# Kernel tuning notes

Hardware: AMD Instinct MI355X
Metric: run time of the kernel (lower is better)

## Reference

```python
import jax, jax.numpy as jnp
import numpy as np

K = 32  # neighbors per query point


def _gather_points(x, idx):
    # x: [B, N, D], idx: [B, M, k] -> [B, M, k, D]
    B, M, k = idx.shape
    D = x.shape[-1]
    flat = jnp.take_along_axis(x, idx.reshape(B, M * k, 1), axis=1)
    return flat.reshape(B, M, k, D)


def setup_inputs() -> dict:
    key = jax.random.key(0)
    k1, k2, k3, k4, k5 = jax.random.split(key, 5)
    B, N, M, Cin = 16, 4096, 1024, 64
    pos = jax.random.normal(k1, (B, N, 3), dtype=jnp.float32)
    features = jax.random.normal(k2, (B, N, Cin), dtype=jnp.float32)
    idx = jax.random.randint(k3, (B, M), 0, N, dtype=jnp.int64)
    # 1x1 conv2d MLP params: (Cin+3) -> 64 -> 128 (use_xyz adds 3 channels)
    W1 = jax.random.normal(k4, (Cin + 3, 64), dtype=jnp.float32) * (1.0 / np.sqrt(Cin + 3))
    b1 = jnp.zeros((64,), dtype=jnp.float32)
    W2 = jax.random.normal(k5, (64, 128), dtype=jnp.float32) * (1.0 / np.sqrt(64))
    b2 = jnp.zeros((128,), dtype=jnp.float32)
    return {"pos": pos, "features": features, "W1": W1, "b1": b1,
            "W2": W2, "b2": b2, "idx": idx}


def reference(pos, features, W1, b1, W2, b2, idx):
    # pos: [B,N,3], features: [B,N,C], idx: [B,M] query-point indices
    pos_q = jnp.take_along_axis(pos, idx[..., None], axis=1)  # [B,M,3]
    # squared-distance knn: [B,M,N]
    d2 = (jnp.sum(pos_q ** 2, -1, keepdims=True)
          + jnp.sum(pos ** 2, -1)[:, None, :]
          - 2.0 * jnp.einsum("bmd,bnd->bmn", pos_q, pos))
    _, nn_idx = jax.lax.top_k(-d2, K)  # [B,M,K] nearest neighbors
    grouped_pos = _gather_points(pos, nn_idx)          # [B,M,K,3]
    grouped_feat = _gather_points(features, nn_idx)    # [B,M,K,C]
    rel = grouped_pos - pos_q[:, :, None, :]           # recenter groups
    x = jnp.concatenate([rel, grouped_feat], axis=-1)  # [B,M,K,C+3] (use_xyz)
    # 1x1 conv2d MLP == per-point linear + ReLU on channel dim
    h = jax.nn.relu(jnp.einsum("bmkc,cd->bmkd", x, W1) + b1)
    h = jax.nn.relu(jnp.einsum("bmkc,cd->bmkd", h, W2) + b2)
    out = jnp.max(h, axis=-2)  # max over K neighbors -> [B,M,128]
    return (pos_q, out)
```

## Files before the change

kernel.cpp:

```cpp
#include <hip/hip_runtime.h>

#define NPTS  4096
#define MQ    1024
#define BATCH 16
#define KNN   32
#define CIN   64
#define H1D   64
#define H2D   128

typedef _Float16 half8 __attribute__((ext_vector_type(8)));
typedef float    floatx4 __attribute__((ext_vector_type(4)));

#define WS_NN_BYTES ((size_t)BATCH * MQ * KNN * 4)
#define W1F_HALVES  (3 * 4 * 64 * 8)
#define W2F_HALVES  (2 * 8 * 64 * 8)
#define WS_P4_OFF   (WS_NN_BYTES + (W1F_HALVES + W2F_HALVES) * 2)

__global__ __launch_bounds__(256) void wprep_kernel(
    const float* __restrict__ W1, const float* __restrict__ W2,
    const float* __restrict__ pos,
    _Float16* __restrict__ wout, float4* __restrict__ pos4)
{
    const int gid = blockIdx.x * 256 + threadIdx.x;
    if (gid < 768) {
        const int s = gid;
        const int kc = s >> 8, nt = (s >> 6) & 3, lane = s & 63;
        const int col = lane & 15, quad = lane >> 4;
        half8 ph;
#pragma unroll
        for (int j = 0; j < 8; ++j) {
            const int k = kc * 32 + quad * 8 + j;
            ph[j] = (k < 67) ? (_Float16)W1[k * H1D + nt * 16 + col] : (_Float16)0.0f;
        }
        *(half8*)(wout + (size_t)s * 8) = ph;
    } else if (gid < 1792) {
        const int s2 = gid - 768;
        const int kc2 = s2 >> 9, nt2 = (s2 >> 6) & 7, lane = s2 & 63;
        const int col = lane & 15, quad = lane >> 4;
        half8 ph;
#pragma unroll
        for (int j = 0; j < 8; ++j) {
            const int k = kc2 * 32 + quad * 8 + j;
            ph[j] = (_Float16)W2[k * H2D + nt2 * 16 + col];
        }
        *(half8*)(wout + (size_t)W1F_HALVES + (size_t)s2 * 8) = ph;
    } else {
        const int p = gid - 1792;
        if (p < BATCH * NPTS) {
            const float px = pos[p * 3 + 0], py = pos[p * 3 + 1], pz = pos[p * 3 + 2];
            float4 v;
            v.x = px; v.y = py; v.z = pz;
            v.w = __fadd_rn(__fadd_rn(__fmul_rn(px, px), __fmul_rn(py, py)),
                            __fmul_rn(pz, pz));
            pos4[p] = v;
        }
    }
}

__global__ __launch_bounds__(256, 4) void knn_kernel(
    const float4* __restrict__ pos4, const int* __restrict__ idx,
    float* __restrict__ pos_q, int* __restrict__ nn)
{
    const int bid = blockIdx.x;
    const int b   = bid >> 10;
    const int m   = bid & (MQ - 1);
    const int t   = threadIdx.x;
    const int wv  = t >> 6, lane = t & 63;

    __shared__ __align__(16) unsigned int hist[1024];
    __shared__ unsigned int wred[8];
    __shared__ unsigned int wsum[4];
    __shared__ unsigned int sc[8];
    __shared__ unsigned int ckey[64];
    __shared__ int          cidx[64];
    __shared__ int          outidx[KNN];

    const float4* pb4 = pos4 + (size_t)b * NPTS;
    const int qn = idx[(size_t)b * MQ + m];
    const float4 qv = pb4[qn];
    const float qq = qv.w;

    *(uint4*)&hist[t * 4] = make_uint4(0u, 0u, 0u, 0u);

    float4 p[16];
#pragma unroll
    for (int i = 0; i < 16; ++i) p[i] = pb4[i * 256 + t];

    unsigned int k[16];
    unsigned int lmin = 0xFFFFFFFFu, lmax = 0u;
#pragma unroll
    for (int i = 0; i < 16; ++i) {
        const float qp = __fadd_rn(__fadd_rn(__fmul_rn(qv.x, p[i].x), __fmul_rn(qv.y, p[i].y)),
                                   __fmul_rn(qv.z, p[i].z));
        const float d2 = __fsub_rn(__fadd_rn(qq, p[i].w), __fmul_rn(2.0f, qp));
        unsigned int u = __float_as_uint(d2);
        u = (u & 0x80000000u) ? ~u : (u | 0x80000000u);
        k[i] = u;
        lmin = min(lmin, u);
        lmax = max(lmax, u);
    }
#pragma unroll
    for (int off = 32; off; off >>= 1) {
        lmin = min(lmin, (unsigned int)__shfl_xor(lmin, off));
        lmax = max(lmax, (unsigned int)__shfl_xor(lmax, off));
    }
    if (lane == 0) { wred[wv] = lmin; wred[4 + wv] = lmax; }
    __syncthreads();
    const unsigned int umin = min(min(wred[0], wred[1]), min(wred[2], wred[3]));
    const unsigned int umax = max(max(wred[4], wred[5]), max(wred[6], wred[7]));
    const unsigned int rng  = umax - umin;
#pragma unroll
    for (int i = 0; i < 16; ++i) k[i] -= umin;

    int sCur;
    {
        const int bits = (rng == 0u) ? 0 : (32 - __clz(rng));
        sCur = (bits > 10) ? (bits - 10) : 0;
    }

#pragma unroll
    for (int i = 0; i < 16; ++i) atomicAdd(&hist[k[i] >> sCur], 1u);
    __syncthreads();

    unsigned int prefix = 0u, rank = KNN - 1;
    int bcnt = 0, nb = 0;
    bool first = true;
    for (;;) {
        const uint4 c4 = *(const uint4*)&hist[t * 4];
        const unsigned int ssum = c4.x + c4.y + c4.z + c4.w;
        unsigned int v = ssum;
#pragma unroll
        for (int off = 1; off < 64; off <<= 1) {
            const unsigned int o = __shfl_up(v, off);
            if (lane >= off) v += o;
        }
        if (lane == 63) wsum[wv] = v;
        __syncthreads();
        unsigned int woff = 0;
        for (int i = 0; i < wv; ++i) woff += wsum[i];
        const unsigned int incl = woff + v, excl = incl - ssum;
        if (rank >= excl && rank < incl) {
            const unsigned int cnt[4] = {c4.x, c4.y, c4.z, c4.w};
            unsigned int e = excl;
            for (int j = 0; j < 4; ++j) {
                if (rank < e + cnt[j]) {
                    sc[0] = (unsigned int)(t * 4 + j);
                    sc[1] = rank - e;
                    sc[2] = cnt[j];
                    break;
                }
                e += cnt[j];
            }
        }
        __syncthreads();
        const unsigned int bin = sc[0];
        rank = sc[1];
        bcnt = (int)sc[2];
        prefix = first ? bin : ((prefix << nb) | bin);
        first = false;
        if (bcnt <= 64 || sCur == 0) break;

        const int sNext = (sCur > 10) ? (sCur - 10) : 0;
        nb = sCur - sNext;
        __syncthreads();
        *(uint4*)&hist[t * 4] = make_uint4(0u, 0u, 0u, 0u);
        __syncthreads();
        const unsigned int mask = (1u << nb) - 1u;
#pragma unroll
        for (int i = 0; i < 16; ++i) {
            if ((k[i] >> sCur) == prefix)
                atomicAdd(&hist[(k[i] >> sNext) & mask], 1u);
        }
        __syncthreads();
        sCur = sNext;
    }

    if (t == 0) { sc[3] = 0u; sc[4] = 0u; }
    __syncthreads();
#pragma unroll
    for (int i = 0; i < 16; ++i) {
        const unsigned int hp = k[i] >> sCur;
        if (hp < prefix) {
            outidx[atomicAdd(&sc[3], 1u)] = i * 256 + t;
        } else if (hp == prefix) {
            const unsigned int slot = atomicAdd(&sc[4], 1u);
            if (slot < 64u) { ckey[slot] = k[i]; cidx[slot] = i * 256 + t; }
        }
    }
    __syncthreads();
    const int defcnt  = (int)sc[3];
    const int candcnt = min((int)sc[4], 64);

    if (wv == 0) {
        const unsigned int k_l = (lane < candcnt) ? ckey[lane] : 0xFFFFFFFFu;
        const int          i_l = (lane < candcnt) ? cidx[lane] : 0x7FFFFFFF;
        int rk = 0;
        for (int j = 0; j < candcnt; ++j) {
            const unsigned int kj = __shfl(k_l, j);
            const int          ij = __shfl(i_l, j);
            if (kj < k_l || (kj == k_l && ij < i_l)) ++rk;
        }
        if (lane < candcnt && rk <= (int)rank) outidx[defcnt + rk] = i_l;
    }
    __syncthreads();
    if (t < KNN) nn[(size_t)bid * KNN + t] = outidx[t];
    if (t == 0) {
        pos_q[(size_t)bid * 3 + 0] = qv.x;
        pos_q[(size_t)bid * 3 + 1] = qv.y;
        pos_q[(size_t)bid * 3 + 2] = qv.z;
    }
}

__global__ __launch_bounds__(256, 4) void mlp_kernel(
    const float4* __restrict__ pos4, const float* __restrict__ feat,
    const float* __restrict__ b1, const float* __restrict__ b2,
    const float* __restrict__ pos_q, const int* __restrict__ nn,
    const _Float16* __restrict__ wf, float* __restrict__ out)
{
    __shared__ _Float16 sh[4 * 3072];
    const int t = threadIdx.x;
    const int w = t >> 6, lane = t & 63;
    const int col = lane & 15, quad = lane >> 4;
    const int q = blockIdx.x * 4 + w;
    const int b = q >> 10;
    const int wbase = w * 3072;

    {
        const int r = t >> 1, h = t & 1;
        const int kk = r & 31;
        const int n = nn[(size_t)q * KNN + kk];
        const float4 pv = pos4[(size_t)b * NPTS + n];
        const float4* f4 = (const float4*)(feat + ((size_t)b * NPTS + n) * CIN);
        const int mt = kk >> 4, lrow = kk & 15;
        if (h == 0) {
            float4 ff[12];
#pragma unroll
            for (int ii = 0; ii < 12; ++ii) ff[ii] = f4[ii];
            float rel[3];
            rel[0] = pv.x - pos_q[(size_t)q * 3 + 0];
            rel[1] = pv.y - pos_q[(size_t)q * 3 + 1];
            rel[2] = pv.z - pos_q[(size_t)q * 3 + 2];
#pragma unroll
            for (int ci = 0; ci < 6; ++ci) {
                half8 ph;
#pragma unroll
                for (int jj = 0; jj < 8; ++jj) {
                    const int c = ci * 8 + jj;
                    float v;
                    if (c < 3) v = rel[c];
                    else {
                        const int fc = c - 3;
                        const float4 vv = ff[fc >> 2];
                        v = ((fc & 3) == 0) ? vv.x : ((fc & 3) == 1) ? vv.y
                          : ((fc & 3) == 2) ? vv.z : vv.w;
                    }
                    ph[jj] = (_Float16)v;
                }
                const int kc = ci >> 2, qd = ci & 3;
                *(half8*)&sh[wbase + ((kc * 2 + mt) * 64 + qd * 16 + lrow) * 8] = ph;
            }
        } else {
            float4 ff[5];
#pragma unroll
            for (int ii = 0; ii < 5; ++ii) ff[ii] = f4[11 + ii];
#pragma unroll
            for (int ci = 6; ci < 12; ++ci) {
                half8 ph;
#pragma unroll
                for (int jj = 0; jj < 8; ++jj) {
                    const int c = ci * 8 + jj;
                    float v = 0.0f;
                    if (c < 67) {
                        const int fc = c - 3;
                        const float4 vv = ff[(fc >> 2) - 11];
                        v = ((fc & 3) == 0) ? vv.x : ((fc & 3) == 1) ? vv.y
                          : ((fc & 3) == 2) ? vv.z : vv.w;
                    }
                    ph[jj] = (_Float16)v;
                }
                const int kc = ci >> 2, qd = ci & 3;
                *(half8*)&sh[wbase + ((kc * 2 + mt) * 64 + qd * 16 + lrow) * 8] = ph;
            }
        }
    }

    half8 af[3][2];
#pragma unroll
    for (int kc = 0; kc < 3; ++kc)
#pragma unroll
        for (int mt = 0; mt < 2; ++mt)
            af[kc][mt] = *(const half8*)&sh[wbase + ((kc * 2 + mt) * 64 + lane) * 8];

    half8 w1f[3][4];
#pragma unroll
    for (int kc = 0; kc < 3; ++kc)
#pragma unroll
        for (int nt = 0; nt < 4; ++nt)
            w1f[kc][nt] = *(const half8*)(wf + (size_t)((kc * 4 + nt) * 64 + lane) * 8);

#pragma unroll
    for (int nt = 0; nt < 4; ++nt) {
        const float bv = b1[nt * 16 + col];
        floatx4 acc0 = {bv, bv, bv, bv}, acc1 = acc0;
#pragma unroll
        for (int kc = 0; kc < 3; ++kc) {
            acc0 = __builtin_amdgcn_mfma_f32_16x16x32_f16(af[kc][0], w1f[kc][nt], acc0, 0, 0, 0);
            acc1 = __builtin_amdgcn_mfma_f32_16x16x32_f16(af[kc][1], w1f[kc][nt], acc1, 0, 0, 0);
        }
        const int kc2 = nt >> 1;
        const int quad2 = (((nt & 1) * 16) + col) >> 3;
        const int j2 = col & 7;
#pragma unroll
        for (int mt = 0; mt < 2; ++mt) {
            const floatx4 a = mt ? acc1 : acc0;
#pragma unroll
            for (int reg = 0; reg < 4; ++reg) {
                const int row = quad * 4 + reg;
                sh[wbase + ((kc2 * 2 + mt) * 64 + quad2 * 16 + row) * 8 + j2] =
                    (_Float16)fmaxf(a[reg], 0.0f);
            }
        }
    }

    half8 a2[2][2];
#pragma unroll
    for (int kc2 = 0; kc2 < 2; ++kc2)
#pragma unroll
        for (int mt = 0; mt < 2; ++mt)
            a2[kc2][mt] = *(const half8*)&sh[wbase + ((kc2 * 2 + mt) * 64 + lane) * 8];

    half8 w2f[2][8];
#pragma unroll
    for (int kc2 = 0; kc2 < 2; ++kc2)
#pragma unroll
        for (int nt2 = 0; nt2 < 8; ++nt2)
            w2f[kc2][nt2] = *(const half8*)(wf + (size_t)W1F_HALVES
                                            + (size_t)((kc2 * 8 + nt2) * 64 + lane) * 8);

    float* oq = out + (size_t)q * H2D;
#pragma unroll
    for (int nt2 = 0; nt2 < 8; ++nt2) {
        const float bv = b2[nt2 * 16 + col];
        floatx4 acc0 = {bv, bv, bv, bv}, acc1 = acc0;
#pragma unroll
        for (int kc2 = 0; kc2 < 2; ++kc2) {
            acc0 = __builtin_amdgcn_mfma_f32_16x16x32_f16(a2[kc2][0], w2f[kc2][nt2], acc0, 0, 0, 0);
            acc1 = __builtin_amdgcn_mfma_f32_16x16x32_f16(a2[kc2][1], w2f[kc2][nt2], acc1, 0, 0, 0);
        }
        float mm = fmaxf(fmaxf(fmaxf(acc0[0], acc0[1]), fmaxf(acc0[2], acc0[3])),
                         fmaxf(fmaxf(acc1[0], acc1[1]), fmaxf(acc1[2], acc1[3])));
        mm = fmaxf(mm, 0.0f);
        mm = fmaxf(mm, __shfl_xor(mm, 16));
        mm = fmaxf(mm, __shfl_xor(mm, 32));
        if (lane < 16) oq[nt2 * 16 + lane] = mm;
    }
}

extern "C" void kernel_launch(void* const* d_in, const int* in_sizes, int n_in,
                              void* d_out, int out_size, void* d_ws, size_t ws_size,
                              hipStream_t stream)
{
    const float* pos  = (const float*)d_in[0];
    const float* feat = (const float*)d_in[1];
    const float* W1   = (const float*)d_in[2];
    const float* b1   = (const float*)d_in[3];
    const float* W2   = (const float*)d_in[4];
    const float* b2   = (const float*)d_in[5];
    const int*   idx  = (const int*)d_in[6];

    float* pos_q = (float*)d_out;
    float* out   = (float*)d_out + (size_t)BATCH * MQ * 3;
    int*      nn = (int*)d_ws;
    _Float16* wf = (_Float16*)((char*)d_ws + WS_NN_BYTES);
    float4*   p4 = (float4*)((char*)d_ws + WS_P4_OFF);

    const int prep_threads = 1792 + BATCH * NPTS;
    wprep_kernel<<<(prep_threads + 255) / 256, 256, 0, stream>>>(W1, W2, pos, wf, p4);
    knn_kernel<<<BATCH * MQ, 256, 0, stream>>>(p4, idx, pos_q, nn);
    mlp_kernel<<<BATCH * MQ / 4, 256, 0, stream>>>(p4, feat, b1, b2,
                                                   pos_q, nn, wf, out);
}
```

Measured before the change: 190.4 us.

## Pre-pack features to fp16 MFMA rows and load A fragments directly

The prep kernel now converts every point's 64 float features into a padded 96-half fp16 row laid out in MFMA K order, with the xyz slots left zero. The MLP kernel then loads its A fragments straight from global memory by neighbor index, patches in the relative xyz, and no longer stages the input through shared memory. This removes the per-query fp32 gather, the conversion work and an LDS round trip, and shrinks shared memory. In exchange the prep kernel reads all features once and writes a 12.6 MB fp16 buffer, and the gathers become 16-byte accesses that are less coalesced.

```diff
diff --git a/kernel.cpp b/kernel.cpp
--- a/kernel.cpp
+++ b/kernel.cpp
@@ -15,11 +15,14 @@
 #define W1F_HALVES  (3 * 4 * 64 * 8)
 #define W2F_HALVES  (2 * 8 * 64 * 8)
 #define WS_P4_OFF   (WS_NN_BYTES + (W1F_HALVES + W2F_HALVES) * 2)
+#define WS_X16_OFF  (WS_P4_OFF + (size_t)BATCH * NPTS * 16)
+#define XROW        96
 
 __global__ __launch_bounds__(256) void wprep_kernel(
     const float* __restrict__ W1, const float* __restrict__ W2,
-    const float* __restrict__ pos,
-    _Float16* __restrict__ wout, float4* __restrict__ pos4)
+    const float* __restrict__ pos, const float* __restrict__ feat,
+    _Float16* __restrict__ wout, float4* __restrict__ pos4,
+    _Float16* __restrict__ x16)
 {
     const int gid = blockIdx.x * 256 + threadIdx.x;
     if (gid < 768) {
@@ -53,6 +56,29 @@
             v.w = __fadd_rn(__fadd_rn(__fmul_rn(px, px), __fmul_rn(py, py)),
                             __fmul_rn(pz, pz));
             pos4[p] = v;
+
+            const float4* f4 = (const float4*)(feat + (size_t)p * CIN);
+            float4 ff[16];
+#pragma unroll
+            for (int ii = 0; ii < 16; ++ii) ff[ii] = f4[ii];
+            _Float16* xr = x16 + (size_t)p * XROW;
+#pragma unroll
+            for (int ci = 0; ci < 12; ++ci) {
+                half8 ph;
+#pragma unroll
+                for (int jj = 0; jj < 8; ++jj) {
+                    const int c = ci * 8 + jj;
+                    float v2 = 0.0f;
+                    if (c >= 3 && c < 67) {
+                        const int fc = c - 3;
+                        const float4 vv = ff[fc >> 2];
+                        v2 = ((fc & 3) == 0) ? vv.x : ((fc & 3) == 1) ? vv.y
+                           : ((fc & 3) == 2) ? vv.z : vv.w;
+                    }
+                    ph[jj] = (_Float16)v2;
+                }
+                *(half8*)(xr + ci * 8) = ph;
+            }
         }
     }
 }
@@ -212,84 +238,50 @@
 }
 
 __global__ __launch_bounds__(256, 4) void mlp_kernel(
-    const float4* __restrict__ pos4, const float* __restrict__ feat,
+    const float4* __restrict__ pos4, const _Float16* __restrict__ x16,
     const float* __restrict__ b1, const float* __restrict__ b2,
     const float* __restrict__ pos_q, const int* __restrict__ nn,
     const _Float16* __restrict__ wf, float* __restrict__ out)
 {
-    __shared__ _Float16 sh[4 * 3072];
+    __shared__ _Float16 sh[4 * 2048];
     const int t = threadIdx.x;
     const int w = t >> 6, lane = t & 63;
     const int col = lane & 15, quad = lane >> 4;
     const int q = blockIdx.x * 4 + w;
     const int b = q >> 10;
-    const int wbase = w * 3072;
+    const int wbase = w * 2048;
+    const int row = lane & 15;
+
+    const int n0 = nn[(size_t)q * KNN + row];
+    const int n1 = nn[(size_t)q * KNN + 16 + row];
+
+    const _Float16* xb = x16 + (size_t)b * NPTS * XROW;
+    const _Float16* x0 = xb + (size_t)n0 * XROW + quad * 8;
+    const _Float16* x1 = xb + (size_t)n1 * XROW + quad * 8;
+
+    half8 af[3][2];
+    af[0][0] = *(const half8*)(x0);
+    af[1][0] = *(const half8*)(x0 + 32);
+    af[2][0] = *(const half8*)(x0 + 64);
+    af[0][1] = *(const half8*)(x1);
+    af[1][1] = *(const half8*)(x1 + 32);
+    af[2][1] = *(const half8*)(x1 + 64);
 
     {
-        const int r = t >> 1, h = t & 1;
-        const int kk = r & 31;
-        const int n = nn[(size_t)q * KNN + kk];
-        const float4 pv = pos4[(size_t)b * NPTS + n];
-        const float4* f4 = (const float4*)(feat + ((size_t)b * NPTS + n) * CIN);
-        const int mt = kk >> 4, lrow = kk & 15;
-        if (h == 0) {
-            float4 ff[12];
-#pragma unroll
-            for (int ii = 0; ii < 12; ++ii) ff[ii] = f4[ii];
-            float rel[3];
-            rel[0] = pv.x - pos_q[(size_t)q * 3 + 0];
-            rel[1] = pv.y - pos_q[(size_t)q * 3 + 1];
-            rel[2] = pv.z - pos_q[(size_t)q * 3 + 2];
-#pragma unroll
-            for (int ci = 0; ci < 6; ++ci) {
-                half8 ph;
-#pragma unroll
-                for (int jj = 0; jj < 8; ++jj) {
-                    const int c = ci * 8 + jj;
-                    float v;
-                    if (c < 3) v = rel[c];
-                    else {
-                        const int fc = c - 3;
-                        const float4 vv = ff[fc >> 2];
-                        v = ((fc & 3) == 0) ? vv.x : ((fc & 3) == 1) ? vv.y
-                          : ((fc & 3) == 2) ? vv.z : vv.w;
-                    }
-                    ph[jj] = (_Float16)v;
-                }
-                const int kc = ci >> 2, qd = ci & 3;
-                *(half8*)&sh[wbase + ((kc * 2 + mt) * 64 + qd * 16 + lrow) * 8] = ph;
-            }
-        } else {
-            float4 ff[5];
-#pragma unroll
-            for (int ii = 0; ii < 5; ++ii) ff[ii] = f4[11 + ii];
-#pragma unroll
-            for (int ci = 6; ci < 12; ++ci) {
-                half8 ph;
-#pragma unroll
-                for (int jj = 0; jj < 8; ++jj) {
-                    const int c = ci * 8 + jj;
-                    float v = 0.0f;
-                    if (c < 67) {
-                        const int fc = c - 3;
-                        const float4 vv = ff[(fc >> 2) - 11];
-                        v = ((fc & 3) == 0) ? vv.x : ((fc & 3) == 1) ? vv.y
-                          : ((fc & 3) == 2) ? vv.z : vv.w;
-                    }
-                    ph[jj] = (_Float16)v;
-                }
-                const int kc = ci >> 2, qd = ci & 3;
-                *(half8*)&sh[wbase + ((kc * 2 + mt) * 64 + qd * 16 + lrow) * 8] = ph;
-            }
-        }
-    }
-
-    half8 af[3][2];
-#pragma unroll
-    for (int kc = 0; kc < 3; ++kc)
-#pragma unroll
-        for (int mt = 0; mt < 2; ++mt)
-            af[kc][mt] = *(const half8*)&sh[wbase + ((kc * 2 + mt) * 64 + lane) * 8];
+        const float qx = pos_q[(size_t)q * 3 + 0];
+        const float qy = pos_q[(size_t)q * 3 + 1];
+        const float qz = pos_q[(size_t)q * 3 + 2];
+        const float4 pv0 = pos4[(size_t)b * NPTS + n0];
+        const float4 pv1 = pos4[(size_t)b * NPTS + n1];
+        if (quad == 0) {
+            af[0][0][0] = (_Float16)(pv0.x - qx);
+            af[0][0][1] = (_Float16)(pv0.y - qy);
+            af[0][0][2] = (_Float16)(pv0.z - qz);
+            af[0][1][0] = (_Float16)(pv1.x - qx);
+            af[0][1][1] = (_Float16)(pv1.y - qy);
+            af[0][1][2] = (_Float16)(pv1.z - qz);
+        }
+    }
 
     half8 w1f[3][4];
 #pragma unroll
@@ -315,8 +307,8 @@
             const floatx4 a = mt ? acc1 : acc0;
 #pragma unroll
             for (int reg = 0; reg < 4; ++reg) {
-                const int row = quad * 4 + reg;
-                sh[wbase + ((kc2 * 2 + mt) * 64 + quad2 * 16 + row) * 8 + j2] =
+                const int hrow = quad * 4 + reg;
+                sh[wbase + ((kc2 * 2 + mt) * 64 + quad2 * 16 + hrow) * 8 + j2] =
                     (_Float16)fmaxf(a[reg], 0.0f);
             }
         }
@@ -370,13 +362,15 @@
 
     float* pos_q = (float*)d_out;
     float* out   = (float*)d_out + (size_t)BATCH * MQ * 3;
-    int*      nn = (int*)d_ws;
-    _Float16* wf = (_Float16*)((char*)d_ws + WS_NN_BYTES);
-    float4*   p4 = (float4*)((char*)d_ws + WS_P4_OFF);
+    int*       nn  = (int*)d_ws;
+    _Float16*  wf  = (_Float16*)((char*)d_ws + WS_NN_BYTES);
+    float4*    p4  = (float4*)((char*)d_ws + WS_P4_OFF);
+    _Float16*  x16 = (_Float16*)((char*)d_ws + WS_X16_OFF);
 
     const int prep_threads = 1792 + BATCH * NPTS;
-    wprep_kernel<<<(prep_threads + 255) / 256, 256, 0, stream>>>(W1, W2, pos, wf, p4);
+    wprep_kernel<<<(prep_threads + 255) / 256, 256, 0, stream>>>(W1, W2, pos, feat,
+                                                                 wf, p4, x16);
     knn_kernel<<<BATCH * MQ, 256, 0, stream>>>(p4, idx, pos_q, nn);
-    mlp_kernel<<<BATCH * MQ / 4, 256, 0, stream>>>(p4, feat, b1, b2,
+    mlp_kernel<<<BATCH * MQ / 4, 256, 0, stream>>>(p4, x16, b1, b2,
                                                    pos_q, nn, wf, out);
 }
```

Measured after the change: 188.4 us (median of 2 runs). No clear change (-1.0%).
